# Kernel optimization log

Measured on AMD Instinct MI355X. Metric: run time of the kernel, lower is better.

The kernel has to match this reference:

```python
import jax, jax.numpy as jnp
import numpy as np

VOC, EMB, HID = 32000, 512, 1024
B, S = 16, 256


def setup_inputs() -> dict:
    key = jax.random.key(0)
    ks = jax.random.split(key, 12)
    s_e = 1.0 / np.sqrt(HID)
    inp = {
        "inputs": jax.random.randint(ks[0], (B, S), 0, VOC, dtype=jnp.int64),
        "emb": jax.random.normal(ks[1], (VOC, EMB), dtype=jnp.float32),
        "W_ih1": jax.random.uniform(ks[2], (4 * HID, EMB), minval=-s_e, maxval=s_e),
        "W_hh1": jax.random.uniform(ks[3], (4 * HID, HID), minval=-s_e, maxval=s_e),
        "b_ih1": jax.random.uniform(ks[4], (4 * HID,), minval=-s_e, maxval=s_e),
        "b_hh1": jax.random.uniform(ks[5], (4 * HID,), minval=-s_e, maxval=s_e),
        "W_ih2": jax.random.uniform(ks[6], (4 * HID, HID), minval=-s_e, maxval=s_e),
        "W_hh2": jax.random.uniform(ks[7], (4 * HID, HID), minval=-s_e, maxval=s_e),
        "b_ih2": jax.random.uniform(ks[8], (4 * HID,), minval=-s_e, maxval=s_e),
        "b_hh2": jax.random.uniform(ks[9], (4 * HID,), minval=-s_e, maxval=s_e),
        "W_log": jax.random.uniform(ks[10], (VOC, HID), minval=-s_e, maxval=s_e),
        "b_log": jnp.zeros((VOC,), dtype=jnp.float32),  # init_weights zeroes logits bias
    }
    return inp


def _lstm_cell(x, h, c, W_ih, W_hh, b_ih, b_hh):
    # PyTorch LSTMCell: gates ordered (i, f, g, o)
    g = x @ W_ih.T + b_ih + h @ W_hh.T + b_hh  # [B, 4H]
    i, f, gg, o = jnp.split(g, 4, axis=-1)
    c_new = jax.nn.sigmoid(f) * c + jax.nn.sigmoid(i) * jnp.tanh(gg)
    h_new = jax.nn.sigmoid(o) * jnp.tanh(c_new)
    return h_new, c_new


def reference(inputs, emb, W_ih1, W_hh1, b_ih1, b_hh1,
              W_ih2, W_hh2, b_ih2, b_hh2, W_log, b_log):
    # Dropout is evaluated in inference mode (identity), for determinism.
    embed = emb[inputs]  # [B, S, E]
    xs = jnp.swapaxes(embed, 0, 1)  # [S, B, E]
    bsz = inputs.shape[0]
    h1 = jnp.zeros((bsz, HID), embed.dtype)
    c1 = jnp.zeros((bsz, HID), embed.dtype)
    h2 = jnp.zeros((bsz, HID), embed.dtype)
    c2 = jnp.zeros((bsz, HID), embed.dtype)

    def step(carry, x_t):
        h1, c1, h2, c2 = carry
        h1, c1 = _lstm_cell(x_t, h1, c1, W_ih1, W_hh1, b_ih1, b_hh1)
        h2, c2 = _lstm_cell(h1, h2, c2, W_ih2, W_hh2, b_ih2, b_hh2)
        return (h1, c1, h2, c2), h2

    _, hid_seq = jax.lax.scan(step, (h1, c1, h2, c2), xs)  # [S, B, H]
    hid_seq = jnp.swapaxes(hid_seq, 0, 1)  # [B, S, H]
    logits = hid_seq @ W_log.T + b_log  # [B, S, V]
    return jax.nn.log_softmax(logits, axis=-1)
```

## Files before the change

kernel.cpp:

```cpp
#include <hip/hip_runtime.h>
#include <hip/hip_bf16.h>

typedef __attribute__((ext_vector_type(8))) _Float16 half8;
typedef __attribute__((ext_vector_type(4))) _Float16 half4;
typedef __attribute__((ext_vector_type(4))) float f32x4;
typedef __attribute__((ext_vector_type(4))) unsigned int u32x4;

#define VOC 32000
#define EMB 512
#define HID 1024
#define SS  256
#define NROW 4096
#define CHK 43
#define CSTRIDE 64
#define SLOTB (64 * CSTRIDE * 16)
#define NS 4
#define SPIN (1 << 16)
#define ROWH 264
#define SH_TR 30
#define SH_TC 150

__device__ __forceinline__ float sigf(float x) {
    return 1.f / (1.f + __expf(-x));
}
__device__ __forceinline__ float tanh_c(float x) {
    x = fminf(fmaxf(x, -15.f), 15.f);
    float e = __expf(2.f * x);
    return (e - 1.f) / (e + 1.f);
}

__device__ __forceinline__ u32x4 ldg_u4_cc(const void* p) {
    u32x4 r;
    asm volatile("global_load_dwordx4 %0, %1, off sc0 sc1" : "=v"(r) : "v"(p));
    return r;
}
__device__ __forceinline__ void stg_u4_cc(void* p, u32x4 v) {
    asm volatile("global_store_dwordx4 %0, %1, off sc0 sc1" :: "v"(p), "v"(v) : "memory");
}
__device__ __forceinline__ void stg_h8_cc(_Float16* p, half8 v) {
    asm volatile("global_store_dwordx4 %0, %1, off sc0 sc1" :: "v"(p), "v"(v) : "memory");
}
__device__ __forceinline__ void stg_u32_cc(unsigned* p, unsigned v) {
    asm volatile("global_store_dword %0, %1, off sc0 sc1" :: "v"(p), "v"(v) : "memory");
}
__device__ __forceinline__ unsigned ldg_u32_cc(const unsigned* p) {
    unsigned v;
    asm volatile("global_load_dword %0, %1, off sc0 sc1\n\ts_waitcnt vmcnt(0)"
                 : "=v"(v) : "v"(p) : "memory");
    return v;
}
__device__ __forceinline__ half8 to_agpr(half8 v) {
    asm volatile("" : "+a"(v));
    return v;
}
__device__ __forceinline__ void gload16(const void* g, void* lds) {
    __builtin_amdgcn_global_load_lds(
        (const __attribute__((address_space(1))) unsigned int*)(uintptr_t)g,
        (__attribute__((address_space(3))) unsigned int*)(unsigned int)(uintptr_t)lds,
        16, 0, 0);
}

__global__ void k_zero(float* p, int n) {
    int i = blockIdx.x * blockDim.x + threadIdx.x;
    int st = gridDim.x * blockDim.x;
    for (; i < n; i += st) p[i] = 0.f;
}

__global__ void k_cvt_all(const float* __restrict__ s0, const float* __restrict__ s1,
                          const float* __restrict__ s2, const float* __restrict__ s3,
                          const float* __restrict__ s4,
                          _Float16* __restrict__ d0, _Float16* __restrict__ d1,
                          _Float16* __restrict__ d2, _Float16* __restrict__ d3,
                          _Float16* __restrict__ d4) {
    const int n0 = 4096 * 512 / 4;
    const int n1 = 4096 * 1024 / 4;
    const int n4 = VOC * 1024 / 4;
    const int nT = n0 + 3 * n1 + n4;
    int i = blockIdx.x * 256 + threadIdx.x;
    int st = gridDim.x * 256;
    for (; i < nT; i += st) {
        const float* s; _Float16* d; int k = i;
        if (k < n0) { s = s0; d = d0; }
        else {
            k -= n0;
            if (k < n1) { s = s1; d = d1; }
            else {
                k -= n1;
                if (k < n1) { s = s2; d = d2; }
                else {
                    k -= n1;
                    if (k < n1) { s = s3; d = d3; }
                    else { k -= n1; s = s4; d = d4; }
                }
            }
        }
        float4 v = ((const float4*)s)[k];
        half4 o = {(_Float16)v.x, (_Float16)v.y, (_Float16)v.z, (_Float16)v.w};
        ((half4*)d)[k] = o;
    }
}

__global__ void k_bias(const float* bi1, const float* bh1,
                       const float* bi2, const float* bh2,
                       float* b1, float* b2) {
    int i = blockIdx.x * blockDim.x + threadIdx.x;
    if (i < 4 * HID) { b1[i] = bi1[i] + bh1[i]; b2[i] = bi2[i] + bh2[i]; }
}

__global__ void k_embed(const int* __restrict__ tok, const float* __restrict__ emb,
                        _Float16* __restrict__ A) {
    int idx = blockIdx.x * 256 + threadIdx.x;
    if (idx >= NROW * (EMB / 4)) return;
    int r = idx >> 7, c4 = idx & 127;
    int t = r >> 4, b = r & 15;
    int token = tok[b * SS + t];
    float4 v = ((const float4*)(emb + (size_t)token * EMB))[c4];
    half4 o = {(_Float16)v.x, (_Float16)v.y, (_Float16)v.z, (_Float16)v.w};
    ((half4*)(A + (size_t)r * EMB))[c4] = o;
}

template <int F16OUT>
__global__ __launch_bounds__(512, 1) void k_gemm8(
    const _Float16* __restrict__ A, const _Float16* __restrict__ B,
    const float* __restrict__ bias, float* __restrict__ Cf,
    _Float16* __restrict__ Ch, int M, int N, int K, int scatter,
    int rowOff, int colOff) {
    __shared__ __align__(16) char smem[131072];
    int tid = threadIdx.x;
    int wave = tid >> 6, lane = tid & 63;
    int wm = wave >> 2, wn = wave & 3;
    int nbx = gridDim.x;
    int lin = blockIdx.y * nbx + blockIdx.x;
    {
        int n = nbx * gridDim.y;
        if ((n & 7) == 0) { int cpx = n >> 3; lin = (lin & 7) * cpx + (lin >> 3); }
    }
    int bRow = rowOff + (lin / nbx) * 256, bCol = colOff + (lin % nbx) * 256;
    int nt = K >> 6;
    int lrow = lane & 15, kq = lane >> 4;

    auto stage = [&](int mat, int h, int t) {
        const _Float16* src = mat ? B : A;
        int r0 = mat ? bCol : bRow;
        char* dst = smem + (size_t)(t & 1) * 65536 + mat * 32768 + h * 16384;
#pragma unroll
        for (int j = 0; j < 2; ++j) {
            int ci = j * 512 + tid;
            int row = ci >> 3, slot = ci & 7;
            int grow = h * 128 + row;
            int gsl = slot ^ (row & 7);
            gload16(src + (size_t)(r0 + grow) * K + t * 64 + gsl * 8, dst + ci * 16);
        }
    };
    auto rdA = [&](int bf, int mi, int kk) -> half8 {
        int r = wm * 128 + mi * 16 + lrow;
        int sl = (kk * 4 + kq) ^ (lrow & 7);
        return *(const half8*)(smem + (size_t)bf * 65536 + r * 128 + sl * 16);
    };
    auto rdB = [&](int bf, int ni, int kk) -> half8 {
        int r = wn * 64 + ni * 16 + lrow;
        int sl = (kk * 4 + kq) ^ (lrow & 7);
        return *(const half8*)(smem + (size_t)bf * 65536 + 32768 + r * 128 + sl * 16);
    };

    f32x4 acc[8][4] = {};

    stage(1, 0, 0); stage(0, 0, 0); stage(1, 1, 0); stage(0, 1, 0);
    if (nt > 1) { stage(1, 0, 1); stage(0, 0, 1); }

    for (int u = 0; u < nt; ++u) {
        int bf = u & 1;
        if (u + 1 == nt) asm volatile("s_waitcnt vmcnt(0)" ::: "memory");
        else             asm volatile("s_waitcnt vmcnt(4)" ::: "memory");
        __builtin_amdgcn_s_barrier();
        __builtin_amdgcn_sched_barrier(0);
        if (u + 1 < nt) stage(1, 1, u + 1);
        half8 a[8][2], b[4][2];
#pragma unroll
        for (int mi = 0; mi < 8; ++mi)
#pragma unroll
            for (int kk = 0; kk < 2; ++kk)
                a[mi][kk] = rdA(bf, mi, kk);
#pragma unroll
        for (int ni = 0; ni < 4; ++ni)
#pragma unroll
            for (int kk = 0; kk < 2; ++kk)
                b[ni][kk] = rdB(bf, ni, kk);
        __builtin_amdgcn_s_setprio(1);
#pragma unroll
        for (int mi = 0; mi < 8; ++mi)
#pragma unroll
            for (int ni = 0; ni < 4; ++ni) {
                acc[mi][ni] = __builtin_amdgcn_mfma_f32_16x16x32_f16(a[mi][0], b[ni][0], acc[mi][ni], 0, 0, 0);
                acc[mi][ni] = __builtin_amdgcn_mfma_f32_16x16x32_f16(a[mi][1], b[ni][1], acc[mi][ni], 0, 0, 0);
            }
        __builtin_amdgcn_s_setprio(0);
        asm volatile("s_waitcnt lgkmcnt(0)" ::: "memory");
        __builtin_amdgcn_s_barrier();
        __builtin_amdgcn_sched_barrier(0);
        if (u + 1 < nt) stage(0, 1, u + 1);
        if (u + 2 < nt) { stage(1, 0, u + 2); stage(0, 0, u + 2); }
    }

    float bv[4];
#pragma unroll
    for (int ni = 0; ni < 4; ++ni)
        bv[ni] = bias[bCol + wn * 64 + ni * 16 + lrow];
#pragma unroll
    for (int mi = 0; mi < 8; ++mi)
#pragma unroll
        for (int ni = 0; ni < 4; ++ni)
#pragma unroll
            for (int q = 0; q < 4; ++q) {
                int gr = bRow + wm * 128 + mi * 16 + kq * 4 + q;
                int gc = bCol + wn * 64 + ni * 16 + lrow;
                float v = acc[mi][ni][q] + bv[ni];
                size_t orow = scatter ? (size_t)(((gr & 15) << 8) | (gr >> 4)) : (size_t)gr;
                if (F16OUT) Ch[orow * (size_t)N + gc] = (_Float16)v;
                else        Cf[orow * (size_t)N + gc] = v;
            }
}

__device__ __forceinline__ void poll_stage2(const char* base, int exp, int cnt,
                                            unsigned short* hs, int sbp, int r) {
    u32x4 cv[11];
#pragma unroll
    for (int j = 0; j < 11; ++j)
        if (j < cnt) cv[j] = ldg_u4_cc(base + j * 64);
    for (int it = 0; it < SPIN; ++it) {
        asm volatile("s_waitcnt vmcnt(0)" ::: "memory");
        __builtin_amdgcn_sched_barrier(0);
        bool bad = false;
#pragma unroll
        for (int j = 0; j < 11; ++j)
            if (j < cnt && (int)cv[j][3] < exp) {
                cv[j] = ldg_u4_cc(base + j * 64);
                bad = true;
            }
        if (!bad) break;
        __builtin_amdgcn_s_sleep(1);
    }
#pragma unroll
    for (int j = 0; j < 11; ++j)
        if (j < cnt) {
            int c = r + 4 * j;
            unsigned* dst = (unsigned*)((char*)hs + sbp * (2 * ROWH) + c * 12);
            dst[0] = cv[j][0]; dst[1] = cv[j][1]; dst[2] = cv[j][2];
        }
}

__global__ __launch_bounds__(256, 1) void k_fused(
    const _Float16* __restrict__ X,
    const _Float16* __restrict__ Whh1, const _Float16* __restrict__ Wih2,
    const _Float16* __restrict__ Whh2, const float* __restrict__ b2s,
    char* __restrict__ h1buf, char* __restrict__ h2buf,
    unsigned* __restrict__ prog, _Float16* __restrict__ h2seq,
    const _Float16* __restrict__ Wlog, const float* __restrict__ blog,
    _Float16* __restrict__ logh) {
    __shared__ __align__(16) char smem[84992];
    int tid = threadIdx.x;
    int bid = blockIdx.x;

    if (bid >= 128) {
        _Float16* As = (_Float16*)smem;
        _Float16* Bs = (_Float16*)(smem + 8192);
        int wave = tid >> 6, lane = tid & 63;
        int wr = (wave >> 1) * 64, wc = (wave & 1) * 64;
        int lrow = lane & 15, khalf = (lane >> 4) * 8;
        int lcol = lane & 15, lrow4 = (lane >> 4) * 4;
        int pcg = -1;
        for (int idx = bid - 128; idx < SH_TR * SH_TC; idx += 128) {
            int tr = idx / SH_TC, tc = idx % SH_TC;
            int needed = tr * 8 + 12;
            if (pcg < needed) {
                if (tid < 64) {
                    const unsigned* pp = prog + (size_t)(64 + tid) * 16;
                    for (int it = 0; it < SPIN; ++it) {
                        unsigned v = ldg_u32_cc(pp);
                        if ((int)v >= needed) break;
                        __builtin_amdgcn_s_sleep(16);
                    }
                }
                __syncthreads();
                pcg = needed;
            }
            int bRow = tr * 128, bCol = tc * 128;
            f32x4 acc[4][4] = {};
            for (int kt = 0; kt < HID; kt += 32) {
#pragma unroll
                for (int q = 0; q < 2; ++q) {
                    int ci = q * 256 + wave * 64 + lane;
                    int row = ci >> 2, c8 = (ci & 3) * 8;
                    int ldsoff = (q * 256 + wave * 64) * 16;
                    gload16(h2seq + (size_t)(bRow + row) * HID + kt + c8, (char*)As + ldsoff);
                    gload16(Wlog + (size_t)(bCol + row) * HID + kt + c8, (char*)Bs + ldsoff);
                }
                __syncthreads();
                half8 a[4], b[4];
#pragma unroll
                for (int i = 0; i < 4; ++i)
                    a[i] = *(const half8*)(&As[(wr + 16 * i + lrow) * 32 + khalf]);
#pragma unroll
                for (int j = 0; j < 4; ++j)
                    b[j] = *(const half8*)(&Bs[(wc + 16 * j + lrow) * 32 + khalf]);
#pragma unroll
                for (int i = 0; i < 4; ++i)
#pragma unroll
                    for (int j = 0; j < 4; ++j)
                        acc[i][j] = __builtin_amdgcn_mfma_f32_16x16x32_f16(a[i], b[j], acc[i][j], 0, 0, 0);
                __syncthreads();
            }
#pragma unroll
            for (int i = 0; i < 4; ++i)
#pragma unroll
                for (int j = 0; j < 4; ++j)
#pragma unroll
                    for (int q = 0; q < 4; ++q) {
                        int gr = bRow + wr + 16 * i + lrow4 + q;
                        int gc = bCol + wc + 16 * j + lcol;
                        size_t orow = (size_t)(((gr & 15) << 8) | (gr >> 4));
                        logh[orow * (size_t)VOC + gc] = (_Float16)(acc[i][j][q] + blog[gc]);
                    }
        }
        return;
    }

    unsigned short* hsPA = (unsigned short*)smem;
    unsigned short* hsPB = (unsigned short*)(smem + 33792);
    float* gsp = (float*)(smem + 67584);
    unsigned short* hstage = (unsigned short*)(smem + 83968);
    int w = tid >> 6, l = tid & 63;
    int layer = bid >> 6, sb = bid & 63;
    int sbp = tid >> 2, r = tid & 3;
    int cnt = (r == 3) ? 10 : 11;
    size_t choff = (size_t)(sbp * CSTRIDE + r) * 16;
    int hp = l >> 5;
    int hoff = (l & 15) * 16 + ((l >> 4) & 1) * 8;

    half8 wA[32];
    half8 wB[32];
    {
        const _Float16* base = layer ? Wih2 : Whh1;
        const _Float16* wp = base + (size_t)(w * HID + sb * 16 + (l & 15)) * HID + (l >> 4) * 8;
#pragma unroll
        for (int kt = 0; kt < 32; ++kt)
            wA[kt] = to_agpr(*(const half8*)(wp + kt * 32));
        if (layer) {
            const _Float16* wq = Whh2 + (size_t)(w * HID + sb * 16 + (l & 15)) * HID + (l >> 4) * 8;
#pragma unroll
            for (int kt = 0; kt < 32; ++kt)
                wB[kt] = to_agpr(*(const half8*)(wq + kt * 32));
        }
    }
    float bias_v = layer ? b2s[w * HID + sb * 16 + (l & 15)] : 0.f;

    int eb = tid >> 4, ecol = tid & 15;
    int gidx = ((eb >> 2) * 16 + ecol) * 4 + (eb & 3);
    float creg = 0.f;
    int pc = 0;

    if (!layer) {
        const _Float16* xbase = X + (size_t)w * HID + sb * 16 + (l & 15);
        int bq = (l >> 4) * 4;
        f32x4 xreg;
        {
            const _Float16* xp = xbase + (size_t)bq * 4096;
            xreg[0] = (float)xp[0]; xreg[1] = (float)xp[4096];
            xreg[2] = (float)xp[8192]; xreg[3] = (float)xp[12288];
        }
        for (int g = 0; g < SS; ++g) {
            int tn = (g + 1 < SS) ? g + 1 : SS - 1;
            const _Float16* xp = xbase + (size_t)(tn * 16 + bq) * 4096;
            float xn0 = (float)xp[0], xn1 = (float)xp[4096],
                  xn2 = (float)xp[8192], xn3 = (float)xp[12288];

            poll_stage2(h1buf + ((g - 1) & 3) * SLOTB + choff, g, cnt, hsPA, sbp, r);
            __syncthreads();
            if (tid == 0) stg_u32_cc(prog + (size_t)bid * 16, (unsigned)(g + 1));

            f32x4 a0 = xreg, a1 = {}, a2 = {}, a3 = {};
#pragma unroll
            for (int c = 0; c < 4; ++c) {
                half8 ha[8];
#pragma unroll
                for (int j = 0; j < 8; ++j)
                    ha[j] = *(const half8*)(hsPA + (2 * (c * 8 + j) + hp) * ROWH + hoff);
#pragma unroll
                for (int j = 0; j < 8; ++j) {
                    f32x4* ac = (j & 3) == 0 ? &a0 : (j & 3) == 1 ? &a1 : (j & 3) == 2 ? &a2 : &a3;
                    *ac = __builtin_amdgcn_mfma_f32_16x16x32_f16(ha[j], wA[c * 8 + j], *ac, 0, 0, 0);
                }
            }
            a0 = (a0 + a1) + (a2 + a3);

            *(f32x4*)(&gsp[w * 1024 + l * 4]) = a0;
            __syncthreads();

            float gi = gsp[gidx], gf = gsp[1024 + gidx],
                  gg = gsp[2048 + gidx], go = gsp[3072 + gidx];
            float cn = sigf(gf) * creg + sigf(gi) * tanh_c(gg);
            float hn = sigf(go) * tanh_c(cn);
            creg = cn;
            _Float16 hh = (_Float16)hn;
            unsigned short hu;
            __builtin_memcpy(&hu, &hh, 2);
            hstage[eb * 16 + ecol] = hu;
            xreg[0] = xn0; xreg[1] = xn1; xreg[2] = xn2; xreg[3] = xn3;
            __syncthreads();

            if (tid < 128 && pc < g - 2) {
                const unsigned* pp = prog + (size_t)tid * 16;
                for (int it = 0; it < SPIN; ++it) {
                    unsigned v = ldg_u32_cc(pp);
                    if ((int)v >= g - 2) { pc = (int)v; break; }
                    __builtin_amdgcn_s_sleep(1);
                }
            }
            __syncthreads();
            if (w == 0 && l < CHK) {
                const unsigned* hsu = (const unsigned*)hstage;
                u32x4 pv;
                pv[0] = hsu[l * 3]; pv[1] = hsu[l * 3 + 1]; pv[2] = hsu[l * 3 + 2];
                pv[3] = (unsigned)(g + 1);
                stg_u4_cc(h1buf + (g & 3) * SLOTB + (size_t)(sb * CSTRIDE + l) * 16, pv);
            }
        }
    } else {
        for (int s = 0; s < SS; ++s) {
            poll_stage2(h2buf + ((s - 1) & 3) * SLOTB + choff, s, cnt, hsPB, sbp, r);
            poll_stage2(h1buf + (s & 3) * SLOTB + choff, s + 1, cnt, hsPA, sbp, r);
            __syncthreads();
            if (tid == 0) stg_u32_cc(prog + (size_t)bid * 16, (unsigned)(s + 1));

            f32x4 a0 = {bias_v, bias_v, bias_v, bias_v}, a1 = {}, a2 = {}, a3 = {};
#pragma unroll
            for (int c = 0; c < 4; ++c) {
                half8 ha[8];
#pragma unroll
                for (int j = 0; j < 8; ++j)
                    ha[j] = *(const half8*)(hsPB + (2 * (c * 8 + j) + hp) * ROWH + hoff);
#pragma unroll
                for (int j = 0; j < 8; ++j) {
                    f32x4* ac = (j & 3) == 0 ? &a0 : (j & 3) == 1 ? &a1 : (j & 3) == 2 ? &a2 : &a3;
                    *ac = __builtin_amdgcn_mfma_f32_16x16x32_f16(ha[j], wB[c * 8 + j], *ac, 0, 0, 0);
                }
            }
#pragma unroll
            for (int c = 0; c < 4; ++c) {
                half8 ha[8];
#pragma unroll
                for (int j = 0; j < 8; ++j)
                    ha[j] = *(const half8*)(hsPA + (2 * (c * 8 + j) + hp) * ROWH + hoff);
#pragma unroll
                for (int j = 0; j < 8; ++j) {
                    f32x4* ac = (j & 3) == 0 ? &a0 : (j & 3) == 1 ? &a1 : (j & 3) == 2 ? &a2 : &a3;
                    *ac = __builtin_amdgcn_mfma_f32_16x16x32_f16(ha[j], wA[c * 8 + j], *ac, 0, 0, 0);
                }
            }
            a0 = (a0 + a1) + (a2 + a3);

            *(f32x4*)(&gsp[w * 1024 + l * 4]) = a0;
            __syncthreads();

            float gi = gsp[gidx], gf = gsp[1024 + gidx],
                  gg = gsp[2048 + gidx], go = gsp[3072 + gidx];
            float cn = sigf(gf) * creg + sigf(gi) * tanh_c(gg);
            float hn = sigf(go) * tanh_c(cn);
            creg = cn;
            _Float16 hh = (_Float16)hn;
            unsigned short hu;
            __builtin_memcpy(&hu, &hh, 2);
            hstage[eb * 16 + ecol] = hu;
            __syncthreads();

            if (tid < 64 && pc < s - 2) {
                const unsigned* pp = prog + (size_t)(64 + tid) * 16;
                for (int it = 0; it < SPIN; ++it) {
                    unsigned v = ldg_u32_cc(pp);
                    if ((int)v >= s - 2) { pc = (int)v; break; }
                    __builtin_amdgcn_s_sleep(1);
                }
            }
            __syncthreads();
            if (w == 0 && l < CHK) {
                const unsigned* hsu = (const unsigned*)hstage;
                u32x4 pv;
                pv[0] = hsu[l * 3]; pv[1] = hsu[l * 3 + 1]; pv[2] = hsu[l * 3 + 2];
                pv[3] = (unsigned)(s + 1);
                stg_u4_cc(h2buf + (s & 3) * SLOTB + (size_t)(sb * CSTRIDE + l) * 16, pv);
            }
            if (w == 1 && l < 32) {
                half8 hv = *(const half8*)((const char*)hstage + l * 16);
                stg_h8_cc(h2seq + (size_t)(s * 16 + (l >> 1)) * HID + sb * 16 + (l & 1) * 8, hv);
            }
        }
    }
}

__global__ __launch_bounds__(320) void k_lsm_f(float* __restrict__ logits) {
    int r = blockIdx.x, tid = threadIdx.x;
    float* row = logits + (size_t)r * VOC;
    f32x4 v[25];
    float m = -3.4e38f;
#pragma unroll
    for (int j = 0; j < 25; ++j) {
        v[j] = ((const f32x4*)row)[tid + 320 * j];
        m = fmaxf(fmaxf(fmaxf(m, v[j][0]), fmaxf(v[j][1], v[j][2])), v[j][3]);
    }
#pragma unroll
    for (int off = 1; off < 64; off <<= 1) m = fmaxf(m, __shfl_xor(m, off));
    __shared__ float sm[5], ssum[5];
    int wv = tid >> 6;
    if ((tid & 63) == 0) sm[wv] = m;
    __syncthreads();
    m = fmaxf(fmaxf(fmaxf(sm[0], sm[1]), fmaxf(sm[2], sm[3])), sm[4]);
    float s = 0.f;
#pragma unroll
    for (int j = 0; j < 25; ++j)
        s += (__expf(v[j][0] - m) + __expf(v[j][1] - m)) +
             (__expf(v[j][2] - m) + __expf(v[j][3] - m));
#pragma unroll
    for (int off = 1; off < 64; off <<= 1) s += __shfl_xor(s, off);
    if ((tid & 63) == 0) ssum[wv] = s;
    __syncthreads();
    s = (ssum[0] + ssum[1]) + (ssum[2] + ssum[3]) + ssum[4];
    float lse = m + __logf(s);
#pragma unroll
    for (int j = 0; j < 25; ++j) {
        f32x4 o = v[j];
        o[0] -= lse; o[1] -= lse; o[2] -= lse; o[3] -= lse;
        ((f32x4*)row)[tid + 320 * j] = o;
    }
}

__global__ __launch_bounds__(320) void k_lsm_h(const _Float16* __restrict__ lg,
                                               float* __restrict__ out) {
    int r = blockIdx.x, tid = threadIdx.x;
    const half4* row = (const half4*)(lg + (size_t)r * VOC);
    float* orow = out + (size_t)r * VOC;
    half4 v[25];
    float m = -3.4e38f;
#pragma unroll
    for (int j = 0; j < 25; ++j) {
        v[j] = row[tid + 320 * j];
        float a = (float)v[j][0], b = (float)v[j][1], c = (float)v[j][2], d = (float)v[j][3];
        m = fmaxf(fmaxf(fmaxf(m, a), fmaxf(b, c)), d);
    }
#pragma unroll
    for (int off = 1; off < 64; off <<= 1) m = fmaxf(m, __shfl_xor(m, off));
    __shared__ float sm[5], ssum[5];
    int wv = tid >> 6;
    if ((tid & 63) == 0) sm[wv] = m;
    __syncthreads();
    m = fmaxf(fmaxf(fmaxf(sm[0], sm[1]), fmaxf(sm[2], sm[3])), sm[4]);
    float s = 0.f;
#pragma unroll
    for (int j = 0; j < 25; ++j)
        s += (__expf((float)v[j][0] - m) + __expf((float)v[j][1] - m)) +
             (__expf((float)v[j][2] - m) + __expf((float)v[j][3] - m));
#pragma unroll
    for (int off = 1; off < 64; off <<= 1) s += __shfl_xor(s, off);
    if ((tid & 63) == 0) ssum[wv] = s;
    __syncthreads();
    s = (ssum[0] + ssum[1]) + (ssum[2] + ssum[3]) + ssum[4];
    float lse = m + __logf(s);
#pragma unroll
    for (int j = 0; j < 25; ++j) {
        f32x4 o = {(float)v[j][0] - lse, (float)v[j][1] - lse,
                   (float)v[j][2] - lse, (float)v[j][3] - lse};
        ((f32x4*)orow)[tid + 320 * j] = o;
    }
}

extern "C" void kernel_launch(void* const* d_in, const int* in_sizes, int n_in,
                              void* d_out, int out_size, void* d_ws, size_t ws_size,
                              hipStream_t stream) {
    const int*   tok   = (const int*)d_in[0];
    const float* emb   = (const float*)d_in[1];
    const float* W_ih1 = (const float*)d_in[2];
    const float* W_hh1 = (const float*)d_in[3];
    const float* b_ih1 = (const float*)d_in[4];
    const float* b_hh1 = (const float*)d_in[5];
    const float* W_ih2 = (const float*)d_in[6];
    const float* W_hh2 = (const float*)d_in[7];
    const float* b_ih2 = (const float*)d_in[8];
    const float* b_hh2 = (const float*)d_in[9];
    const float* W_log = (const float*)d_in[10];
    const float* b_log = (const float*)d_in[11];
    float* out = (float*)d_out;

    char* w = (char*)d_ws;
    auto alloc = [&](size_t bytes) {
        char* p = w;
        w += (bytes + 255) & ~(size_t)255;
        return p;
    };
    _Float16* Wih1h = (_Float16*)alloc((size_t)4096 * 512 * 2);
    _Float16* Whh1h = (_Float16*)alloc((size_t)4096 * 1024 * 2);
    _Float16* Wih2h = (_Float16*)alloc((size_t)4096 * 1024 * 2);
    _Float16* Whh2h = (_Float16*)alloc((size_t)4096 * 1024 * 2);
    _Float16* Wlogh = (_Float16*)alloc((size_t)VOC * 1024 * 2);
    _Float16* Abuf  = (_Float16*)alloc((size_t)4096 * 512 * 2);
    _Float16* Xh    = (_Float16*)alloc((size_t)4096 * 4096 * 2);
    _Float16* h2seq = (_Float16*)alloc((size_t)4096 * 1024 * 2);
    float* b1s      = (float*)alloc(4096 * 4);
    float* b2s      = (float*)alloc(4096 * 4);
    char* h1buf     = alloc(NS * SLOTB);
    char* h2buf     = alloc(NS * SLOTB);
    unsigned* prog  = (unsigned*)alloc(128 * 64);
    size_t need = (size_t)(w - (char*)d_ws) + (size_t)NROW * VOC * 2;
    _Float16* logh = (need <= ws_size) ? (_Float16*)alloc((size_t)NROW * VOC * 2) : nullptr;

    k_zero<<<64, 256, 0, stream>>>((float*)h1buf, (2 * NS * SLOTB + 128 * 64) / 4);

    k_cvt_all<<<2048, 256, 0, stream>>>(W_ih1, W_hh1, W_ih2, W_hh2, W_log,
                                        Wih1h, Whh1h, Wih2h, Whh2h, Wlogh);
    k_bias<<<16, 256, 0, stream>>>(b_ih1, b_hh1, b_ih2, b_hh2, b1s, b2s);

    k_embed<<<2048, 256, 0, stream>>>(tok, emb, Abuf);
    k_gemm8<1><<<dim3(16, 16), 512, 0, stream>>>(Abuf, Wih1h, b1s, nullptr, Xh,
                                                 4096, 4096, 512, 0, 0, 0);

    if (logh) {
        k_fused<<<256, 256, 0, stream>>>(Xh, Whh1h, Wih2h, Whh2h, b2s,
                                         h1buf, h2buf, prog, h2seq,
                                         Wlogh, b_log, logh);
        k_gemm8<1><<<dim3(50, 16), 512, 0, stream>>>(h2seq, Wlogh, b_log, nullptr,
                                                     logh, 4096, VOC, 1024, 1,
                                                     0, 19200);
        k_gemm8<1><<<dim3(75, 1), 512, 0, stream>>>(h2seq, Wlogh, b_log, nullptr,
                                                    logh, 4096, VOC, 1024, 1,
                                                    3840, 0);
        k_lsm_h<<<4096, 320, 0, stream>>>(logh, out);
    } else {
        k_fused<<<128, 256, 0, stream>>>(Xh, Whh1h, Wih2h, Whh2h, b2s,
                                         h1buf, h2buf, prog, h2seq,
                                         Wlogh, b_log, nullptr);
        k_gemm8<0><<<dim3(VOC / 256, 16), 512, 0, stream>>>(h2seq, Wlogh, b_log,
                                                            out, nullptr,
                                                            4096, VOC, 1024, 1, 0, 0);
        k_lsm_f<<<4096, 320, 0, stream>>>(out);
    }
}
```

Baseline: 1.532 ms.

## Compute entire logits GEMM in fused kernel via atomic work-stealing queue

```diff
diff --git a/kernel.cpp b/kernel.cpp
--- a/kernel.cpp
+++ b/kernel.cpp
@@ -17,8 +17,7 @@
 #define NS 4
 #define SPIN (1 << 16)
 #define ROWH 264
-#define SH_TR 30
-#define SH_TC 150
+#define NTILE (32 * 250)
 
 __device__ __forceinline__ float sigf(float x) {
     return 1.f / (1.f + __expf(-x));
@@ -249,6 +248,102 @@
         }
 }
 
+__device__ __forceinline__ void gemm_ws(
+    const _Float16* __restrict__ h2seq, const _Float16* __restrict__ Wlog,
+    const float* __restrict__ blog, _Float16* __restrict__ logh,
+    unsigned* prog2, unsigned* wq, char* smem, int tid) {
+    int wave = tid >> 6, lane = tid & 63;
+    int wr = (wave >> 1) * 64, wc = (wave & 1) * 64;
+    int lrow = lane & 15, kq = lane >> 4;
+    int lrow4 = (lane >> 4) * 4;
+    volatile int* tsh = (int*)(smem + 84960);
+    int pcg = -1;
+    for (;;) {
+        __syncthreads();
+        if (tid == 0) *tsh = (int)atomicAdd(wq, 1u);
+        __syncthreads();
+        int idx = *tsh;
+        if (idx >= NTILE) break;
+        int tr = idx / 250, tc = idx - tr * 250;
+        int needed = tr * 8 + 8;
+        if (pcg < needed) {
+            if (tid < 64) {
+                const unsigned* pp = prog2 + (size_t)tid * 16;
+                for (int it = 0; it < SPIN; ++it) {
+                    unsigned v = ldg_u32_cc(pp);
+                    if ((int)v >= needed) break;
+                    __builtin_amdgcn_s_sleep(16);
+                }
+            }
+            __syncthreads();
+            pcg = needed;
+        }
+        int bRow = tr * 128, bCol = tc * 128;
+        auto stage = [&](int u) {
+            int bf = u & 1;
+#pragma unroll
+            for (int j = 0; j < 2; ++j) {
+                int ci = j * 256 + tid;
+                int row = ci >> 2, sl = ci & 3;
+                int gsl = (sl ^ (row & 3)) * 8;
+                char* basep = smem + bf * 16384 + (j * 256 + wave * 64) * 16;
+                gload16(h2seq + (size_t)(bRow + row) * HID + u * 32 + gsl, basep);
+                gload16(Wlog + (size_t)(bCol + row) * HID + u * 32 + gsl,
+                        basep + 8192);
+            }
+        };
+        auto rdA = [&](int bf, int i) -> half8 {
+            int r = wr + 16 * i + lrow;
+            int p = kq ^ (r & 3);
+            return *(const half8*)(smem + bf * 16384 + r * 64 + p * 16);
+        };
+        auto rdB = [&](int bf, int j) -> half8 {
+            int r = wc + 16 * j + lrow;
+            int p = kq ^ (r & 3);
+            return *(const half8*)(smem + bf * 16384 + 8192 + r * 64 + p * 16);
+        };
+        f32x4 acc[4][4] = {};
+        stage(0);
+        for (int u = 0; u < 32; ++u) {
+            if (u + 1 < 32) {
+                stage(u + 1);
+                asm volatile("s_waitcnt vmcnt(4)" ::: "memory");
+            } else {
+                asm volatile("s_waitcnt vmcnt(0)" ::: "memory");
+            }
+            __builtin_amdgcn_s_barrier();
+            __builtin_amdgcn_sched_barrier(0);
+            int bf = u & 1;
+            half8 a[4], b[4];
+#pragma unroll
+            for (int i = 0; i < 4; ++i) a[i] = rdA(bf, i);
+#pragma unroll
+            for (int j = 0; j < 4; ++j) b[j] = rdB(bf, j);
+            __builtin_amdgcn_s_setprio(1);
+#pragma unroll
+            for (int i = 0; i < 4; ++i)
+#pragma unroll
+                for (int j = 0; j < 4; ++j)
+                    acc[i][j] = __builtin_amdgcn_mfma_f32_16x16x32_f16(a[i], b[j], acc[i][j], 0, 0, 0);
+            __builtin_amdgcn_s_setprio(0);
+            asm volatile("s_waitcnt lgkmcnt(0)" ::: "memory");
+            __builtin_amdgcn_s_barrier();
+            __builtin_amdgcn_sched_barrier(0);
+        }
+#pragma unroll
+        for (int i = 0; i < 4; ++i)
+#pragma unroll
+            for (int j = 0; j < 4; ++j)
+#pragma unroll
+                for (int q = 0; q < 4; ++q) {
+                    int gr = bRow + wr + 16 * i + lrow4 + q;
+                    int gc = bCol + wc + 16 * j + lrow;
+                    size_t orow = (size_t)(((gr & 15) << 8) | (gr >> 4));
+                    logh[orow * (size_t)VOC + gc] = (_Float16)(acc[i][j][q] + blog[gc]);
+                }
+    }
+}
+
 __global__ __launch_bounds__(256, 1) void k_fused(
     const _Float16* __restrict__ X,
     const _Float16* __restrict__ Whh1, const _Float16* __restrict__ Wih2,
@@ -260,68 +355,11 @@
     __shared__ __align__(16) char smem[84992];
     int tid = threadIdx.x;
     int bid = blockIdx.x;
+    unsigned* prog2 = prog + 2048;
+    unsigned* wq = prog + 3072;
 
     if (bid >= 128) {
-        _Float16* As = (_Float16*)smem;
-        _Float16* Bs = (_Float16*)(smem + 8192);
-        int wave = tid >> 6, lane = tid & 63;
-        int wr = (wave >> 1) * 64, wc = (wave & 1) * 64;
-        int lrow = lane & 15, khalf = (lane >> 4) * 8;
-        int lcol = lane & 15, lrow4 = (lane >> 4) * 4;
-        int pcg = -1;
-        for (int idx = bid - 128; idx < SH_TR * SH_TC; idx += 128) {
-            int tr = idx / SH_TC, tc = idx % SH_TC;
-            int needed = tr * 8 + 12;
-            if (pcg < needed) {
-                if (tid < 64) {
-                    const unsigned* pp = prog + (size_t)(64 + tid) * 16;
-                    for (int it = 0; it < SPIN; ++it) {
-                        unsigned v = ldg_u32_cc(pp);
-                        if ((int)v >= needed) break;
-                        __builtin_amdgcn_s_sleep(16);
-                    }
-                }
-                __syncthreads();
-                pcg = needed;
-            }
-            int bRow = tr * 128, bCol = tc * 128;
-            f32x4 acc[4][4] = {};
-            for (int kt = 0; kt < HID; kt += 32) {
-#pragma unroll
-                for (int q = 0; q < 2; ++q) {
-                    int ci = q * 256 + wave * 64 + lane;
-                    int row = ci >> 2, c8 = (ci & 3) * 8;
-                    int ldsoff = (q * 256 + wave * 64) * 16;
-                    gload16(h2seq + (size_t)(bRow + row) * HID + kt + c8, (char*)As + ldsoff);
-                    gload16(Wlog + (size_t)(bCol + row) * HID + kt + c8, (char*)Bs + ldsoff);
-                }
-                __syncthreads();
-                half8 a[4], b[4];
-#pragma unroll
-                for (int i = 0; i < 4; ++i)
-                    a[i] = *(const half8*)(&As[(wr + 16 * i + lrow) * 32 + khalf]);
-#pragma unroll
-                for (int j = 0; j < 4; ++j)
-                    b[j] = *(const half8*)(&Bs[(wc + 16 * j + lrow) * 32 + khalf]);
-#pragma unroll
-                for (int i = 0; i < 4; ++i)
-#pragma unroll
-                    for (int j = 0; j < 4; ++j)
-                        acc[i][j] = __builtin_amdgcn_mfma_f32_16x16x32_f16(a[i], b[j], acc[i][j], 0, 0, 0);
-                __syncthreads();
-            }
-#pragma unroll
-            for (int i = 0; i < 4; ++i)
-#pragma unroll
-                for (int j = 0; j < 4; ++j)
-#pragma unroll
-                    for (int q = 0; q < 4; ++q) {
-                        int gr = bRow + wr + 16 * i + lrow4 + q;
-                        int gc = bCol + wc + 16 * j + lcol;
-                        size_t orow = (size_t)(((gr & 15) << 8) | (gr >> 4));
-                        logh[orow * (size_t)VOC + gc] = (_Float16)(acc[i][j][q] + blog[gc]);
-                    }
-        }
+        gemm_ws(h2seq, Wlog, blog, logh, prog2, wq, smem, tid);
         return;
     }
 
@@ -346,10 +384,10 @@
         for (int kt = 0; kt < 32; ++kt)
             wA[kt] = to_agpr(*(const half8*)(wp + kt * 32));
         if (layer) {
-            const _Float16* wq = Whh2 + (size_t)(w * HID + sb * 16 + (l & 15)) * HID + (l >> 4) * 8;
+            const _Float16* wq2 = Whh2 + (size_t)(w * HID + sb * 16 + (l & 15)) * HID + (l >> 4) * 8;
 #pragma unroll
             for (int kt = 0; kt < 32; ++kt)
-                wB[kt] = to_agpr(*(const half8*)(wq + kt * 32));
+                wB[kt] = to_agpr(*(const half8*)(wq2 + kt * 32));
         }
     }
     float bias_v = layer ? b2s[w * HID + sb * 16 + (l & 15)] : 0.f;
@@ -431,6 +469,7 @@
             poll_stage2(h1buf + (s & 3) * SLOTB + choff, s + 1, cnt, hsPA, sbp, r);
             __syncthreads();
             if (tid == 0) stg_u32_cc(prog + (size_t)bid * 16, (unsigned)(s + 1));
+            if (tid == 1) stg_u32_cc(prog + 2048 + (size_t)sb * 16, (unsigned)s);
 
             f32x4 a0 = {bias_v, bias_v, bias_v, bias_v}, a1 = {}, a2 = {}, a3 = {};
 #pragma unroll
@@ -494,6 +533,14 @@
                 stg_h8_cc(h2seq + (size_t)(s * 16 + (l >> 1)) * HID + sb * 16 + (l & 1) * 8, hv);
             }
         }
+        asm volatile("s_waitcnt vmcnt(0)" ::: "memory");
+        __syncthreads();
+        if (tid == 0) stg_u32_cc(prog + 2048 + (size_t)sb * 16, 256u);
+    }
+
+    if (logh) {
+        __syncthreads();
+        gemm_ws(h2seq, Wlog, blog, logh, prog2, wq, smem, tid);
     }
 }
 
@@ -607,11 +654,11 @@
     float* b2s      = (float*)alloc(4096 * 4);
     char* h1buf     = alloc(NS * SLOTB);
     char* h2buf     = alloc(NS * SLOTB);
-    unsigned* prog  = (unsigned*)alloc(128 * 64);
+    unsigned* prog  = (unsigned*)alloc(12544);
     size_t need = (size_t)(w - (char*)d_ws) + (size_t)NROW * VOC * 2;
     _Float16* logh = (need <= ws_size) ? (_Float16*)alloc((size_t)NROW * VOC * 2) : nullptr;
 
-    k_zero<<<64, 256, 0, stream>>>((float*)h1buf, (2 * NS * SLOTB + 128 * 64) / 4);
+    k_zero<<<64, 256, 0, stream>>>((float*)h1buf, (2 * NS * SLOTB + 12544) / 4);
 
     k_cvt_all<<<2048, 256, 0, stream>>>(W_ih1, W_hh1, W_ih2, W_hh2, W_log,
                                         Wih1h, Whh1h, Wih2h, Whh2h, Wlogh);
@@ -625,12 +672,6 @@
         k_fused<<<256, 256, 0, stream>>>(Xh, Whh1h, Wih2h, Whh2h, b2s,
                                          h1buf, h2buf, prog, h2seq,
                                          Wlogh, b_log, logh);
-        k_gemm8<1><<<dim3(50, 16), 512, 0, stream>>>(h2seq, Wlogh, b_log, nullptr,
-                                                     logh, 4096, VOC, 1024, 1,
-                                                     0, 19200);
-        k_gemm8<1><<<dim3(75, 1), 512, 0, stream>>>(h2seq, Wlogh, b_log, nullptr,
-                                                    logh, 4096, VOC, 1024, 1,
-                                                    3840, 0);
         k_lsm_h<<<4096, 320, 0, stream>>>(logh, out);
     } else {
         k_fused<<<128, 256, 0, stream>>>(Xh, Whh1h, Wih2h, Whh2h, b2s,
```

Measured after the change: 1.417 ms. 7.5% less time.
